# Kernel optimization log

Measured on AMD Instinct MI355X. Metric: run time of the kernel, lower is better.

Reference implementation:

```python
import jax, jax.numpy as jnp
import numpy as np

N, E, DIN, H, D = 100000, 1600000, 256, 4, 32  # nodes, edges, in_feats, heads, out_feats
NEG_SLOPE = 0.2


def setup_inputs() -> dict:
    key = jax.random.key(0)
    ks = jax.random.split(key, 6)
    feat = jax.random.normal(ks[0], (N, DIN), jnp.float32)
    src = jax.random.randint(ks[1], (E,), 0, N, jnp.int32)
    dst = jax.random.randint(ks[2], (E,), 0, N, jnp.int32)
    # fc weight, xavier-normal-ish scale
    W = jax.random.normal(ks[3], (H * D, DIN), jnp.float32) * (2.0 / (DIN + H * D)) ** 0.5
    attn_l = jax.random.normal(ks[4], (1, H, D), jnp.float32) * 0.1
    attn_r = jax.random.normal(ks[5], (1, H, D), jnp.float32) * 0.1
    bias = jnp.zeros((H * D,), jnp.float32)
    return dict(feat=feat, src=src, dst=dst, W=W, attn_l=attn_l, attn_r=attn_r, bias=bias)


def reference(feat, src, dst, W, attn_l, attn_r, bias):
    n = feat.shape[0]
    # node projection: [N, H, D]
    ft = (feat @ W.T).reshape(n, H, D)
    # per-node attention logits: [N, H]
    el = jnp.sum(ft * attn_l, axis=-1)
    er = jnp.sum(ft * attn_r, axis=-1)
    # edge scores (u_add_v + LeakyReLU): [E, H]
    e = jax.nn.leaky_relu(el[src] + er[dst], NEG_SLOPE)
    # segment softmax over incoming edges of each dst node
    m = jax.ops.segment_max(e, dst, num_segments=n)
    m = jnp.where(jnp.isfinite(m), m, 0.0)  # guard zero-in-degree nodes
    ae = jnp.exp(e - m[dst])
    denom = jax.ops.segment_sum(ae, dst, num_segments=n)
    a = ae / denom[dst]  # [E, H]
    # weighted scatter-aggregate (u_mul_e + sum): [N, H, D]
    out = jax.ops.segment_sum(ft[src] * a[:, :, None], dst, num_segments=n)
    return out + bias.reshape(1, H, D)
```

## Files before the change

### kernel.cpp

```cpp
#include <hip/hip_runtime.h>
#include <hip/hip_bf16.h>


#define DIN 256
#define HD 128
#define NEG_SLOPE 0.2f
#define BUCKW 1024
#define BINE 4096

typedef float f32x4 __attribute__((ext_vector_type(4)));
typedef short s16x8 __attribute__((ext_vector_type(8)));

static __device__ __forceinline__ float bf2f(unsigned short u) {
    return __uint_as_float(((unsigned)u) << 16);
}
static __device__ __forceinline__ unsigned short f2bf(float x) {
    unsigned u = __float_as_uint(x);
    unsigned r = (u + 0x7FFFu + ((u >> 16) & 1u)) >> 16;
    return (unsigned short)r;
}

__global__ void transw_kernel(const float* __restrict__ W, unsigned short* __restrict__ Wtb) {
    int idx = blockIdx.x * blockDim.x + threadIdx.x;
    if (idx >= HD * DIN) return;
    int i = idx & 7, c = (idx >> 3) & 127, kb = idx >> 10;
    Wtb[idx] = f2bf(W[(size_t)c * DIN + kb * 8 + i]);
}

__global__ __launch_bounds__(512) void gemm_kernel(
    const float* __restrict__ feat, const unsigned short* __restrict__ Wtb,
    unsigned short* __restrict__ ftu, const float* __restrict__ attn_l,
    const float* __restrict__ attn_r, float* __restrict__ el,
    float* __restrict__ er, int n)
{
    __shared__ unsigned short Bs[32768];
    const int tid = threadIdx.x;
    const int lane = tid & 63;
    const int wv = tid >> 6;
    const int l16 = lane & 15, lq = lane >> 4;
    const int row0 = blockIdx.x * 128 + wv * 16;

    {
        const uint4* s4 = (const uint4*)Wtb;
        uint4* d4 = (uint4*)Bs;
#pragma unroll
        for (int it = 0; it < 8; ++it)
            d4[it * 512 + tid] = s4[it * 512 + tid];
    }
    __syncthreads();

    f32x4 acc[8] = {};
    const int arow = row0 + l16;
    const bool rowok = arow < n;
    const float* fp = feat + (size_t)arow * DIN;
#pragma unroll
    for (int kc = 0; kc < 4; ++kc) {
#pragma unroll
        for (int kk = 0; kk < 2; ++kk) {
            union { s16x8 v; unsigned short u[8]; } au;
            au.v = (s16x8)(short)0;
            if (rowok) {
                const float* ap = fp + kc * 64 + kk * 32 + lq * 8;
                float4 fa = *(const float4*)ap;
                float4 fb = *(const float4*)(ap + 4);
                au.u[0] = f2bf(fa.x); au.u[1] = f2bf(fa.y);
                au.u[2] = f2bf(fa.z); au.u[3] = f2bf(fa.w);
                au.u[4] = f2bf(fb.x); au.u[5] = f2bf(fb.y);
                au.u[6] = f2bf(fb.z); au.u[7] = f2bf(fb.w);
            }
            const int kb = kc * 8 + kk * 4 + lq;
#pragma unroll
            for (int n4 = 0; n4 < 8; ++n4) {
                s16x8 b = *(const s16x8*)&Bs[(kb * 128 + n4 * 16 + l16) * 8];
                acc[n4] = __builtin_amdgcn_mfma_f32_16x16x32_bf16(au.v, b, acc[n4], 0, 0, 0);
            }
        }
    }
#pragma unroll
    for (int n4 = 0; n4 < 8; ++n4)
#pragma unroll
        for (int j = 0; j < 4; ++j) {
            int r = row0 + lq * 4 + j;
            if (r < n) ftu[(size_t)r * HD + n4 * 16 + l16] = f2bf(acc[n4][j]);
        }
    float al8[8], ar8[8];
#pragma unroll
    for (int n4 = 0; n4 < 8; ++n4) {
        al8[n4] = attn_l[n4 * 16 + l16];
        ar8[n4] = attn_r[n4 * 16 + l16];
    }
#pragma unroll
    for (int j = 0; j < 4; ++j) {
        const int r = row0 + lq * 4 + j;
#pragma unroll
        for (int h = 0; h < 4; ++h) {
            float sl = acc[2 * h][j] * al8[2 * h] + acc[2 * h + 1][j] * al8[2 * h + 1];
            float sr = acc[2 * h][j] * ar8[2 * h] + acc[2 * h + 1][j] * ar8[2 * h + 1];
#pragma unroll
            for (int off = 1; off < 16; off <<= 1) {
                sl += __shfl_xor(sl, off);
                sr += __shfl_xor(sr, off);
            }
            if (l16 == ((j << 2) | h) && r < n) {
                el[r * 4 + h] = sl;
                er[r * 4 + h] = sr;
            }
        }
    }
}

__global__ __launch_bounds__(512) void bhist_kernel(
    const int* __restrict__ dst, int* __restrict__ bcnt, int e)
{
    __shared__ int h[128];
    const int tid = threadIdx.x;
    if (tid < 128) h[tid] = 0;
    __syncthreads();
    const int base = blockIdx.x * BINE + tid * 8;
    const int cnt = min(8, max(0, e - base));
    if (cnt == 8) {
        int4 a = *(const int4*)&dst[base];
        int4 b = *(const int4*)&dst[base + 4];
        atomicAdd(&h[a.x >> 10], 1); atomicAdd(&h[a.y >> 10], 1);
        atomicAdd(&h[a.z >> 10], 1); atomicAdd(&h[a.w >> 10], 1);
        atomicAdd(&h[b.x >> 10], 1); atomicAdd(&h[b.y >> 10], 1);
        atomicAdd(&h[b.z >> 10], 1); atomicAdd(&h[b.w >> 10], 1);
    } else {
        for (int m = 0; m < cnt; ++m) atomicAdd(&h[dst[base + m] >> 10], 1);
    }
    __syncthreads();
    if (tid < 128 && h[tid] > 0) atomicAdd(&bcnt[tid], h[tid]);
}

__global__ __launch_bounds__(128) void bscan_kernel(
    const int* __restrict__ bcnt, int* __restrict__ gbase, int* __restrict__ gcur)
{
    __shared__ int ts[128];
    const int tid = threadIdx.x;
    int c = bcnt[tid];
    ts[tid] = c;
    __syncthreads();
#pragma unroll
    for (int off = 1; off < 128; off <<= 1) {
        int v = (tid >= off) ? ts[tid - off] : 0;
        __syncthreads();
        ts[tid] += v;
        __syncthreads();
    }
    gbase[tid] = ts[tid] - c;
    gcur[tid] = ts[tid] - c;
    if (tid == 127) gbase[128] = ts[127];
}

__global__ __launch_bounds__(512) void bin_kernel(
    const int* __restrict__ src, const int* __restrict__ dst,
    int* __restrict__ gcur, unsigned long long* __restrict__ ebuf, int e)
{
    __shared__ int hist[128], lb[128], gb[128], sc[128];
    __shared__ int tot;
    __shared__ unsigned long long pay[BINE];
    const int tid = threadIdx.x;
    if (tid < 128) hist[tid] = 0;
    __syncthreads();
    const int base = blockIdx.x * BINE + tid * 8;
    int sv[8], dv[8], rk[8];
    const int cnt = min(8, max(0, e - base));
    if (cnt == 8) {
        *(int4*)&sv[0] = *(const int4*)&src[base];
        *(int4*)&sv[4] = *(const int4*)&src[base + 4];
        *(int4*)&dv[0] = *(const int4*)&dst[base];
        *(int4*)&dv[4] = *(const int4*)&dst[base + 4];
    } else {
        for (int m = 0; m < cnt; ++m) { sv[m] = src[base + m]; dv[m] = dst[base + m]; }
    }
    for (int m = 0; m < cnt; ++m)
        rk[m] = atomicAdd(&hist[dv[m] >> 10], 1);
    __syncthreads();
    if (tid < 128) sc[tid] = hist[tid];
    __syncthreads();
    for (int off = 1; off < 128; off <<= 1) {
        int v = (tid < 128 && tid >= off) ? sc[tid - off] : 0;
        __syncthreads();
        if (tid < 128) sc[tid] += v;
        __syncthreads();
    }
    if (tid < 128) {
        lb[tid] = sc[tid] - hist[tid];
        if (hist[tid] > 0) gb[tid] = atomicAdd(&gcur[tid], hist[tid]);
    }
    if (tid == 127) tot = sc[127];
    __syncthreads();
    for (int m = 0; m < cnt; ++m) {
        int b = dv[m] >> 10;
        pay[lb[b] + rk[m]] = ((unsigned long long)(unsigned)dv[m] << 32) | (unsigned)sv[m];
    }
    __syncthreads();
    for (int s = tid; s < tot; s += 512) {
        unsigned long long p = pay[s];
        int b = (int)(p >> 42);
        ebuf[gb[b] + (s - lb[b])] = p;
    }
}

__global__ __launch_bounds__(1024) void fine_kernel(
    const unsigned long long* __restrict__ ebuf, const int* __restrict__ gbase,
    int* __restrict__ rowptr, int* __restrict__ srcs_sorted, int n)
{
    __shared__ int deg[1024];
    __shared__ int ts[1024];
    const int b = blockIdx.x, tid = threadIdx.x;
    const int lo = gbase[b], hi = gbase[b + 1];
    const int nbase = b << 10;
    deg[tid] = 0;
    __syncthreads();
    for (int i = lo + tid; i < hi; i += 1024)
        atomicAdd(&deg[((int)(ebuf[i] >> 32)) & 1023], 1);
    __syncthreads();
    const int d = deg[tid];
    ts[tid] = d;
    __syncthreads();
    for (int off = 1; off < 1024; off <<= 1) {
        int v = (tid >= off) ? ts[tid - off] : 0;
        __syncthreads();
        ts[tid] += v;
        __syncthreads();
    }
    const int start = lo + ts[tid] - d;
    if (nbase + tid <= n) rowptr[nbase + tid] = start;
    deg[tid] = start;
    __syncthreads();
    for (int i = lo + tid; i < hi; i += 1024) {
        unsigned long long p = ebuf[i];
        int dd = ((int)(p >> 32)) & 1023;
        int pos = atomicAdd(&deg[dd], 1);
        srcs_sorted[pos] = (int)(unsigned)p;
    }
}

__global__ __launch_bounds__(256) void aggregate_kernel(
    const unsigned short* __restrict__ ftu, const float* __restrict__ el,
    const float* __restrict__ er, const int* __restrict__ rowptr,
    const int* __restrict__ srcs, const float* __restrict__ bias,
    float* __restrict__ out, int n)
{
    __shared__ float plds[4][64][4];
    int v = (int)((blockIdx.x * (unsigned)blockDim.x + threadIdx.x) >> 6);
    if (v >= n) return;
    const int wv = (threadIdx.x >> 6) & 3;
    const int lane = threadIdx.x & 63;
    const int h = lane >> 4;
    const int beg = rowptr[v], end = rowptr[v + 1];
    const float4 er4 = *(const float4*)(er + (size_t)v * 4);
    const uint* __restrict__ ftu32 = (const uint*)ftu;
    float* pl = &plds[wv][0][0];
    float dn = 0.f;
    float acc0 = 0.f, acc1 = 0.f;
    for (int t = beg; t < end; t += 64) {
        const int cnt = min(64, end - t);
        int sj = 0;
        float p0 = 0.f, p1 = 0.f, p2 = 0.f, p3 = 0.f;
        if (lane < cnt) {
            sj = srcs[t + lane];
            float4 elv = *(const float4*)(el + (size_t)sj * 4);
            float e0 = elv.x + er4.x, e1 = elv.y + er4.y;
            float e2 = elv.z + er4.z, e3 = elv.w + er4.w;
            e0 = fmaxf(e0, NEG_SLOPE * e0);
            e1 = fmaxf(e1, NEG_SLOPE * e1);
            e2 = fmaxf(e2, NEG_SLOPE * e2);
            e3 = fmaxf(e3, NEG_SLOPE * e3);
            p0 = __expf(e0); p1 = __expf(e1);
            p2 = __expf(e2); p3 = __expf(e3);
        }
        *(float4*)&pl[lane << 2] = make_float4(p0, p1, p2, p3);
        __builtin_amdgcn_wave_barrier();
        for (int j = 0; j < cnt; j += 16) {
            uint u[16];
            float pj[16];
#pragma unroll
            for (int m = 0; m < 16; ++m) {
                int sjb = __shfl(sj, j + m);
                u[m] = ftu32[(uint)sjb * 64u + (uint)lane];
                pj[m] = pl[((j + m) << 2) + h];
            }
#pragma unroll
            for (int m = 0; m < 16; ++m) {
                dn += pj[m];
                acc0 = fmaf(pj[m], __uint_as_float(u[m] << 16), acc0);
                acc1 = fmaf(pj[m], __uint_as_float(u[m] & 0xffff0000u), acc1);
            }
        }
        __builtin_amdgcn_wave_barrier();
    }
    float inv = dn > 0.f ? 1.f / dn : 0.f;
    float b0 = bias[lane << 1], b1 = bias[(lane << 1) + 1];
    float2 o = make_float2(fmaf(acc0, inv, b0), fmaf(acc1, inv, b1));
    *(float2*)&out[(size_t)v * HD + (lane << 1)] = o;
}

extern "C" void kernel_launch(void* const* d_in, const int* in_sizes, int n_in,
                              void* d_out, int out_size, void* d_ws, size_t ws_size,
                              hipStream_t stream) {
    const float* feat   = (const float*)d_in[0];
    const int*   src    = (const int*)d_in[1];
    const int*   dst    = (const int*)d_in[2];
    const float* W      = (const float*)d_in[3];
    const float* attn_l = (const float*)d_in[4];
    const float* attn_r = (const float*)d_in[5];
    const float* bias   = (const float*)d_in[6];
    float* out = (float*)d_out;
    const int N = in_sizes[0] / DIN;
    const int E = in_sizes[1];
    const int NBUCK = (N + BUCKW - 1) / BUCKW;

    char* w = (char*)d_ws;
    auto alloc = [&](size_t bytes) {
        char* p = w;
        w += (bytes + 255) & ~(size_t)255;
        return p;
    };
    unsigned short* Wtb         = (unsigned short*)alloc((size_t)DIN * HD * 2);
    unsigned short* ftu         = (unsigned short*)alloc((size_t)N * HD * 2);
    float*          el          = (float*)alloc((size_t)N * 4 * 4);
    float*          er          = (float*)alloc((size_t)N * 4 * 4);
    int*            rowptr      = (int*)alloc((size_t)(N + 1) * 4);
    int*            srcs_sorted = (int*)alloc((size_t)E * 4);
    int*            bcnt        = (int*)alloc(128 * 4);
    int*            gbase       = (int*)alloc(129 * 4);
    int*            gcur        = (int*)alloc(128 * 4);
    unsigned long long* ebuf    = (unsigned long long*)alloc((size_t)E * 8);
    (void)ws_size;

    hipMemsetAsync(bcnt, 0, 128 * 4, stream);
    transw_kernel<<<(HD * DIN + 255) / 256, 256, 0, stream>>>(W, Wtb);
    gemm_kernel<<<(N + 127) / 128, 512, 0, stream>>>(feat, Wtb, ftu, attn_l, attn_r, el, er, N);
    bhist_kernel<<<(E + BINE - 1) / BINE, 512, 0, stream>>>(dst, bcnt, E);
    bscan_kernel<<<1, 128, 0, stream>>>(bcnt, gbase, gcur);
    bin_kernel<<<(E + BINE - 1) / BINE, 512, 0, stream>>>(src, dst, gcur, ebuf, E);
    fine_kernel<<<NBUCK, 1024, 0, stream>>>(ebuf, gbase, rowptr, srcs_sorted, N);
    aggregate_kernel<<<(N + 3) / 4, 256, 0, stream>>>(ftu, el, er, rowptr, srcs_sorted, bias, out, N);
}
```

Measured before the change: 174.2 us.

## Fuse weight transpose and dst histogram into GEMM kernel, double rows per block

Removes the separate weight-transpose and histogram kernels. The GEMM blocks now convert W to bf16 straight into LDS, and extra blocks in the same grid compute the dst bucket histogram. Each GEMM block now covers 256 rows, two 16-row tiles per wave, so each B fragment read from LDS feeds two MFMAs. The fine kernel's 1024-wide LDS scan with many barriers is replaced by a wave-shuffle scan plus a small cross-wave prefix. The cost is that every GEMM block redundantly converts the full W, and register pressure rises under launch_bounds(512,4).

```diff
diff --git a/kernel.cpp b/kernel.cpp
--- a/kernel.cpp
+++ b/kernel.cpp
@@ -11,78 +11,99 @@
 typedef float f32x4 __attribute__((ext_vector_type(4)));
 typedef short s16x8 __attribute__((ext_vector_type(8)));
 
-static __device__ __forceinline__ float bf2f(unsigned short u) {
-    return __uint_as_float(((unsigned)u) << 16);
-}
 static __device__ __forceinline__ unsigned short f2bf(float x) {
     unsigned u = __float_as_uint(x);
     unsigned r = (u + 0x7FFFu + ((u >> 16) & 1u)) >> 16;
     return (unsigned short)r;
 }
-
-__global__ void transw_kernel(const float* __restrict__ W, unsigned short* __restrict__ Wtb) {
-    int idx = blockIdx.x * blockDim.x + threadIdx.x;
-    if (idx >= HD * DIN) return;
-    int i = idx & 7, c = (idx >> 3) & 127, kb = idx >> 10;
-    Wtb[idx] = f2bf(W[(size_t)c * DIN + kb * 8 + i]);
-}
-
-__global__ __launch_bounds__(512) void gemm_kernel(
-    const float* __restrict__ feat, const unsigned short* __restrict__ Wtb,
+static __device__ __forceinline__ uint pk2(float a, float b) {
+    return (uint)f2bf(a) | ((uint)f2bf(b) << 16);
+}
+
+__global__ __launch_bounds__(512, 4) void gemm_bhist_kernel(
+    const float* __restrict__ feat, const float* __restrict__ W,
     unsigned short* __restrict__ ftu, const float* __restrict__ attn_l,
     const float* __restrict__ attn_r, float* __restrict__ el,
-    float* __restrict__ er, int n)
+    float* __restrict__ er, int n,
+    const int* __restrict__ dst, int* __restrict__ bcnt, int e, int ngb)
 {
     __shared__ unsigned short Bs[32768];
     const int tid = threadIdx.x;
+
+    if ((int)blockIdx.x >= ngb) {
+        int* h = (int*)Bs;
+        if (tid < 128) h[tid] = 0;
+        __syncthreads();
+        const int base = ((int)blockIdx.x - ngb) * BINE + tid * 8;
+        const int cnt = min(8, max(0, e - base));
+        if (cnt == 8) {
+            int4 a = *(const int4*)&dst[base];
+            int4 b = *(const int4*)&dst[base + 4];
+            atomicAdd(&h[a.x >> 10], 1); atomicAdd(&h[a.y >> 10], 1);
+            atomicAdd(&h[a.z >> 10], 1); atomicAdd(&h[a.w >> 10], 1);
+            atomicAdd(&h[b.x >> 10], 1); atomicAdd(&h[b.y >> 10], 1);
+            atomicAdd(&h[b.z >> 10], 1); atomicAdd(&h[b.w >> 10], 1);
+        } else {
+            for (int m = 0; m < cnt; ++m) atomicAdd(&h[dst[base + m] >> 10], 1);
+        }
+        __syncthreads();
+        if (tid < 128 && h[tid] > 0) atomicAdd(&bcnt[tid], h[tid]);
+        return;
+    }
+
     const int lane = tid & 63;
     const int wv = tid >> 6;
     const int l16 = lane & 15, lq = lane >> 4;
-    const int row0 = blockIdx.x * 128 + wv * 16;
-
-    {
-        const uint4* s4 = (const uint4*)Wtb;
-        uint4* d4 = (uint4*)Bs;
-#pragma unroll
-        for (int it = 0; it < 8; ++it)
-            d4[it * 512 + tid] = s4[it * 512 + tid];
-    }
-    __syncthreads();
-
-    f32x4 acc[8] = {};
-    const int arow = row0 + l16;
-    const bool rowok = arow < n;
-    const float* fp = feat + (size_t)arow * DIN;
+    const int row0 = (int)blockIdx.x * 256 + wv * 32;
+
+#pragma unroll
+    for (int it = 0; it < 8; ++it) {
+        const int cell = it * 512 + tid;
+        const int kb = cell >> 7, c = cell & 127;
+        const float4* wp = (const float4*)&W[(size_t)c * DIN + kb * 8];
+        float4 f0 = wp[0], f1 = wp[1];
+        uint4 pk;
+        pk.x = pk2(f0.x, f0.y); pk.y = pk2(f0.z, f0.w);
+        pk.z = pk2(f1.x, f1.y); pk.w = pk2(f1.z, f1.w);
+        *(uint4*)&Bs[(size_t)cell * 8] = pk;
+    }
+    __syncthreads();
+
+    f32x4 acc[2][8] = {};
+    const int ar0 = row0 + l16, ar1 = row0 + 16 + l16;
+    const bool ok0 = ar0 < n, ok1 = ar1 < n;
+    const float* fp0 = feat + (size_t)ar0 * DIN;
+    const float* fp1 = feat + (size_t)ar1 * DIN;
 #pragma unroll
     for (int kc = 0; kc < 4; ++kc) {
 #pragma unroll
         for (int kk = 0; kk < 2; ++kk) {
-            union { s16x8 v; unsigned short u[8]; } au;
-            au.v = (s16x8)(short)0;
-            if (rowok) {
-                const float* ap = fp + kc * 64 + kk * 32 + lq * 8;
-                float4 fa = *(const float4*)ap;
-                float4 fb = *(const float4*)(ap + 4);
-                au.u[0] = f2bf(fa.x); au.u[1] = f2bf(fa.y);
-                au.u[2] = f2bf(fa.z); au.u[3] = f2bf(fa.w);
-                au.u[4] = f2bf(fb.x); au.u[5] = f2bf(fb.y);
-                au.u[6] = f2bf(fb.z); au.u[7] = f2bf(fb.w);
+            const int koff = kc * 64 + kk * 32 + lq * 8;
+            union { s16x8 v; uint w[4]; } a0, a1;
+            a0.v = (s16x8)(short)0;
+            a1.v = (s16x8)(short)0;
+            if (ok0) {
+                float4 fa = *(const float4*)(fp0 + koff);
+                float4 fb = *(const float4*)(fp0 + koff + 4);
+                a0.w[0] = pk2(fa.x, fa.y); a0.w[1] = pk2(fa.z, fa.w);
+                a0.w[2] = pk2(fb.x, fb.y); a0.w[3] = pk2(fb.z, fb.w);
+            }
+            if (ok1) {
+                float4 fa = *(const float4*)(fp1 + koff);
+                float4 fb = *(const float4*)(fp1 + koff + 4);
+                a1.w[0] = pk2(fa.x, fa.y); a1.w[1] = pk2(fa.z, fa.w);
+                a1.w[2] = pk2(fb.x, fb.y); a1.w[3] = pk2(fb.z, fb.w);
             }
             const int kb = kc * 8 + kk * 4 + lq;
 #pragma unroll
             for (int n4 = 0; n4 < 8; ++n4) {
                 s16x8 b = *(const s16x8*)&Bs[(kb * 128 + n4 * 16 + l16) * 8];
-                acc[n4] = __builtin_amdgcn_mfma_f32_16x16x32_bf16(au.v, b, acc[n4], 0, 0, 0);
-            }
-        }
-    }
-#pragma unroll
-    for (int n4 = 0; n4 < 8; ++n4)
-#pragma unroll
-        for (int j = 0; j < 4; ++j) {
-            int r = row0 + lq * 4 + j;
-            if (r < n) ftu[(size_t)r * HD + n4 * 16 + l16] = f2bf(acc[n4][j]);
-        }
+                acc[0][n4] = __builtin_amdgcn_mfma_f32_16x16x32_bf16(a0.v, b, acc[0][n4], 0, 0, 0);
+                acc[1][n4] = __builtin_amdgcn_mfma_f32_16x16x32_bf16(a1.v, b, acc[1][n4], 0, 0, 0);
+            }
+        }
+    }
+
     float al8[8], ar8[8];
 #pragma unroll
     for (int n4 = 0; n4 < 8; ++n4) {
@@ -90,46 +111,33 @@
         ar8[n4] = attn_r[n4 * 16 + l16];
     }
 #pragma unroll
-    for (int j = 0; j < 4; ++j) {
-        const int r = row0 + lq * 4 + j;
-#pragma unroll
-        for (int h = 0; h < 4; ++h) {
-            float sl = acc[2 * h][j] * al8[2 * h] + acc[2 * h + 1][j] * al8[2 * h + 1];
-            float sr = acc[2 * h][j] * ar8[2 * h] + acc[2 * h + 1][j] * ar8[2 * h + 1];
-#pragma unroll
-            for (int off = 1; off < 16; off <<= 1) {
-                sl += __shfl_xor(sl, off);
-                sr += __shfl_xor(sr, off);
-            }
-            if (l16 == ((j << 2) | h) && r < n) {
-                el[r * 4 + h] = sl;
-                er[r * 4 + h] = sr;
-            }
-        }
-    }
-}
-
-__global__ __launch_bounds__(512) void bhist_kernel(
-    const int* __restrict__ dst, int* __restrict__ bcnt, int e)
-{
-    __shared__ int h[128];
-    const int tid = threadIdx.x;
-    if (tid < 128) h[tid] = 0;
-    __syncthreads();
-    const int base = blockIdx.x * BINE + tid * 8;
-    const int cnt = min(8, max(0, e - base));
-    if (cnt == 8) {
-        int4 a = *(const int4*)&dst[base];
-        int4 b = *(const int4*)&dst[base + 4];
-        atomicAdd(&h[a.x >> 10], 1); atomicAdd(&h[a.y >> 10], 1);
-        atomicAdd(&h[a.z >> 10], 1); atomicAdd(&h[a.w >> 10], 1);
-        atomicAdd(&h[b.x >> 10], 1); atomicAdd(&h[b.y >> 10], 1);
-        atomicAdd(&h[b.z >> 10], 1); atomicAdd(&h[b.w >> 10], 1);
-    } else {
-        for (int m = 0; m < cnt; ++m) atomicAdd(&h[dst[base + m] >> 10], 1);
-    }
-    __syncthreads();
-    if (tid < 128 && h[tid] > 0) atomicAdd(&bcnt[tid], h[tid]);
+    for (int m = 0; m < 2; ++m) {
+#pragma unroll
+        for (int n4 = 0; n4 < 8; ++n4)
+#pragma unroll
+            for (int j = 0; j < 4; ++j) {
+                int r = row0 + m * 16 + lq * 4 + j;
+                if (r < n) ftu[(size_t)r * HD + n4 * 16 + l16] = f2bf(acc[m][n4][j]);
+            }
+#pragma unroll
+        for (int j = 0; j < 4; ++j) {
+            const int r = row0 + m * 16 + lq * 4 + j;
+#pragma unroll
+            for (int h = 0; h < 4; ++h) {
+                float sl = acc[m][2 * h][j] * al8[2 * h] + acc[m][2 * h + 1][j] * al8[2 * h + 1];
+                float sr = acc[m][2 * h][j] * ar8[2 * h] + acc[m][2 * h + 1][j] * ar8[2 * h + 1];
+#pragma unroll
+                for (int off = 1; off < 16; off <<= 1) {
+                    sl += __shfl_xor(sl, off);
+                    sr += __shfl_xor(sr, off);
+                }
+                if (l16 == ((j << 2) | h) && r < n) {
+                    el[r * 4 + h] = sl;
+                    er[r * 4 + h] = sr;
+                }
+            }
+        }
+    }
 }
 
 __global__ __launch_bounds__(128) void bscan_kernel(
@@ -207,8 +215,9 @@
     int* __restrict__ rowptr, int* __restrict__ srcs_sorted, int n)
 {
     __shared__ int deg[1024];
-    __shared__ int ts[1024];
+    __shared__ int wsum[16];
     const int b = blockIdx.x, tid = threadIdx.x;
+    const int lane = tid & 63, wid = tid >> 6;
     const int lo = gbase[b], hi = gbase[b + 1];
     const int nbase = b << 10;
     deg[tid] = 0;
@@ -217,15 +226,21 @@
         atomicAdd(&deg[((int)(ebuf[i] >> 32)) & 1023], 1);
     __syncthreads();
     const int d = deg[tid];
-    ts[tid] = d;
-    __syncthreads();
-    for (int off = 1; off < 1024; off <<= 1) {
-        int v = (tid >= off) ? ts[tid - off] : 0;
-        __syncthreads();
-        ts[tid] += v;
-        __syncthreads();
-    }
-    const int start = lo + ts[tid] - d;
+    int x = d;
+#pragma unroll
+    for (int off = 1; off < 64; off <<= 1) {
+        int y = __shfl(x, lane - off);
+        if (lane >= off) x += y;
+    }
+    if (lane == 63) wsum[wid] = x;
+    __syncthreads();
+    if (tid == 0) {
+        int run = 0;
+#pragma unroll
+        for (int i2 = 0; i2 < 16; ++i2) { int t2 = wsum[i2]; wsum[i2] = run; run += t2; }
+    }
+    __syncthreads();
+    const int start = lo + wsum[wid] + x - d;
     if (nbase + tid <= n) rowptr[nbase + tid] = start;
     deg[tid] = start;
     __syncthreads();
@@ -311,6 +326,8 @@
     const int N = in_sizes[0] / DIN;
     const int E = in_sizes[1];
     const int NBUCK = (N + BUCKW - 1) / BUCKW;
+    const int NGB = (N + 255) / 256;
+    const int EB = (E + BINE - 1) / BINE;
 
     char* w = (char*)d_ws;
     auto alloc = [&](size_t bytes) {
@@ -318,7 +335,6 @@
         w += (bytes + 255) & ~(size_t)255;
         return p;
     };
-    unsigned short* Wtb         = (unsigned short*)alloc((size_t)DIN * HD * 2);
     unsigned short* ftu         = (unsigned short*)alloc((size_t)N * HD * 2);
     float*          el          = (float*)alloc((size_t)N * 4 * 4);
     float*          er          = (float*)alloc((size_t)N * 4 * 4);
@@ -331,11 +347,10 @@
     (void)ws_size;
 
     hipMemsetAsync(bcnt, 0, 128 * 4, stream);
-    transw_kernel<<<(HD * DIN + 255) / 256, 256, 0, stream>>>(W, Wtb);
-    gemm_kernel<<<(N + 127) / 128, 512, 0, stream>>>(feat, Wtb, ftu, attn_l, attn_r, el, er, N);
-    bhist_kernel<<<(E + BINE - 1) / BINE, 512, 0, stream>>>(dst, bcnt, E);
+    gemm_bhist_kernel<<<NGB + EB, 512, 0, stream>>>(
+        feat, W, ftu, attn_l, attn_r, el, er, N, dst, bcnt, E, NGB);
     bscan_kernel<<<1, 128, 0, stream>>>(bcnt, gbase, gcur);
-    bin_kernel<<<(E + BINE - 1) / BINE, 512, 0, stream>>>(src, dst, gcur, ebuf, E);
+    bin_kernel<<<EB, 512, 0, stream>>>(src, dst, gcur, ebuf, E);
     fine_kernel<<<NBUCK, 1024, 0, stream>>>(ebuf, gbase, rowptr, srcs_sorted, N);
     aggregate_kernel<<<(N + 3) / 4, 256, 0, stream>>>(ftu, el, er, rowptr, srcs_sorted, bias, out, N);
 }
```

New measurement: 165.8 us. 1.05x faster.
